# Optimization experiments

Hardware: AMD Instinct MI355X
Metric: run time of the kernel (lower is better)

## Reference

```python
import jax, jax.numpy as jnp
import numpy as np
import math

EPS = 1e-08
KERNEL = 3
PAD = KERNEL // 2


def setup_inputs() -> dict:
    key = jax.random.key(0)
    k1, k2, k3, k4 = jax.random.split(key, 4)
    B, C_in, C_out, H, W, S = 8, 512, 512, 64, 64, 512
    x = jax.random.normal(k1, (B, C_in, H, W), dtype=jnp.float32)
    style = jax.random.normal(k2, (B, S), dtype=jnp.float32)
    # modulation Linear: kaiming_normal fan_in linear => std = 1/sqrt(S); bias filled with 1
    w_mod = jax.random.normal(k3, (C_in, S), dtype=jnp.float32) / math.sqrt(S)
    b_mod = jnp.ones((C_in,), dtype=jnp.float32)
    # conv weight: randn / sqrt(in * k^2)
    weight = jax.random.normal(k4, (1, C_out, C_in, KERNEL, KERNEL), dtype=jnp.float32) / math.sqrt(C_in * KERNEL * KERNEL)
    return {"x": x, "style": style, "w_mod": w_mod, "b_mod": b_mod, "weight": weight}


def _modconv(x, style, w_mod, b_mod, weight):
    # style modulation: (B, S) @ (S, C_in) + bias -> (B, 1, C_in, 1, 1)
    s = style @ w_mod.T + b_mod
    w = weight * s[:, None, :, None, None]            # (B, C_out, C_in, k, k)
    # demodulate: rsqrt of sum of squares over (in, kh, kw)
    demod = jax.lax.rsqrt(jnp.sum(w * w, axis=(2, 3, 4)) + EPS)  # (B, C_out)
    w = w * demod[:, :, None, None, None]

    # groups=B conv == per-sample conv; vmap over batch
    def conv1(xb, wb):
        # xb: (C_in, H, W), wb: (C_out, C_in, k, k)
        return jax.lax.conv_general_dilated(
            xb[None], wb, window_strides=(1, 1),
            padding=[(PAD, PAD), (PAD, PAD)],
            dimension_numbers=("NCHW", "OIHW", "NCHW"))[0]

    return jax.vmap(conv1)(x, w)  # (B, C_out, H, W)


def reference(x, style, w_mod, b_mod, weight):
    return _modconv(x, style, w_mod, b_mod, weight)
```

## Files before the change

### kernel.cpp

```cpp
#include <hip/hip_runtime.h>
#include <hip/hip_bf16.h>

#define BATCH 8
#define CIN   512
#define COUT  512
#define HH    64
#define WW    64
#define SS    512
#define HP    66
#define WP    66
#define NPIX  (HH*WW)

typedef __bf16 bfrag  __attribute__((ext_vector_type(8)));
typedef float  f32x4  __attribute__((ext_vector_type(4)));
typedef unsigned short u16x8 __attribute__((ext_vector_type(8)));

__device__ __forceinline__ void async_copy16(const __hip_bfloat16* g, __hip_bfloat16* l) {
    __builtin_amdgcn_global_load_lds(
        (const __attribute__((address_space(1))) void*)g,
        (__attribute__((address_space(3))) void*)l,
        16, 0, 0);
}

__device__ __forceinline__ bool is_f32(const void* b_mod) {
    return ((const unsigned int*)b_mod)[0] == 0x3F800000u;
}

__global__ void k_prep(const void* __restrict__ style,
                       const void* __restrict__ w_mod,
                       const void* __restrict__ b_mod,
                       const void* __restrict__ weight,
                       float* __restrict__ s_out,
                       float* __restrict__ wsq,
                       __hip_bfloat16* __restrict__ Wt) {
    const bool f32 = is_f32(b_mod);
    if (blockIdx.x < 1024) {
        int tid = blockIdx.x * 256 + threadIdx.x;
        float sq = 0.f;
        if (f32) {
            const float* w = (const float*)weight + (size_t)tid * 9;
#pragma unroll
            for (int k = 0; k < 9; ++k) {
                float v = w[k];
                sq += v * v;
                Wt[k * (COUT * CIN) + tid] = __float2bfloat16(v);
            }
        } else {
            const __hip_bfloat16* w = (const __hip_bfloat16*)weight + (size_t)tid * 9;
#pragma unroll
            for (int k = 0; k < 9; ++k) {
                float v = __bfloat162float(w[k]);
                sq += v * v;
                Wt[k * (COUT * CIN) + tid] = w[k];
            }
        }
        wsq[tid] = sq;
    } else {
        int gw   = (blockIdx.x - 1024) * 4 + (threadIdx.x >> 6);
        int lane = threadIdx.x & 63;
        int b = gw >> 9, i = gw & 511;
        int base = lane * 8;
        float acc = 0.f;
        if (f32) {
            const float* st = (const float*)style + b * SS + base;
            const float* wm = (const float*)w_mod + i * SS + base;
#pragma unroll
            for (int j = 0; j < 8; ++j) acc += st[j] * wm[j];
        } else {
            const __hip_bfloat16* st = (const __hip_bfloat16*)style + b * SS + base;
            const __hip_bfloat16* wm = (const __hip_bfloat16*)w_mod + i * SS + base;
#pragma unroll
            for (int j = 0; j < 8; ++j)
                acc += __bfloat162float(st[j]) * __bfloat162float(wm[j]);
        }
#pragma unroll
        for (int off = 32; off; off >>= 1) acc += __shfl_down(acc, off);
        if (lane == 0) {
            float bias = f32 ? ((const float*)b_mod)[i]
                             : __bfloat162float(((const __hip_bfloat16*)b_mod)[i]);
            s_out[gw] = acc + bias;
        }
    }
}

__global__ void k_mid(const void* __restrict__ xv,
                      const float* __restrict__ s_buf,
                      const float* __restrict__ wsq,
                      const void* __restrict__ b_mod,
                      float* __restrict__ demod,
                      int b0, int nx, int do_demod,
                      __hip_bfloat16* __restrict__ xpad) {
    if ((int)blockIdx.x >= nx) {
        if (!do_demod) return;
        int gw   = ((int)blockIdx.x - nx) * 4 + (threadIdx.x >> 6);
        int lane = threadIdx.x & 63;
        int b = gw >> 9, o = gw & 511;
        int base = lane * 8;
        const float* sp = s_buf + b * CIN + base;
        const float* wp = wsq + o * CIN + base;
        float acc = 0.f;
#pragma unroll
        for (int j = 0; j < 8; ++j) {
            float sv = sp[j];
            acc += sv * sv * wp[j];
        }
#pragma unroll
        for (int off = 32; off; off >>= 1) acc += __shfl_down(acc, off);
        if (lane == 0) demod[gw] = rsqrtf(acc + 1e-8f);
        return;
    }
    const bool f32 = is_f32(b_mod);
    int ic = blockIdx.x & 15;
    int h  = (blockIdx.x >> 4) & 63;
    int bl = blockIdx.x >> 10;
    int b  = b0 + bl;
    int t  = threadIdx.x;
    int g  = t & 3;
    int w  = t >> 2;
    int ch0 = ic * 32 + g * 8;

    float sv[8];
#pragma unroll
    for (int j = 0; j < 8; ++j) sv[j] = s_buf[b * CIN + ch0 + j];

    u16x8 outv;
#pragma unroll
    for (int j = 0; j < 8; ++j) {
        size_t src = (size_t)(b * CIN + ch0 + j) * NPIX + h * WW + w;
        float xval = f32 ? ((const float*)xv)[src]
                         : __bfloat162float(((const __hip_bfloat16*)xv)[src]);
        __hip_bfloat16 bv = __float2bfloat16(xval * sv[j]);
        outv[j] = *(unsigned short*)&bv;
    }
    size_t rowb = (size_t)(bl * HP + h + 1) * WP;
    *(u16x8*)(xpad + (rowb + (w + 1)) * CIN + ch0) = outv;

    u16x8 z = {};
    if (w == 0)  *(u16x8*)(xpad + (rowb + 0)  * CIN + ch0) = z;
    if (w == 63) *(u16x8*)(xpad + (rowb + 65) * CIN + ch0) = z;
    if (h == 0) {
        size_t r0 = (size_t)(bl * HP + 0) * WP;
        *(u16x8*)(xpad + (r0 + (w + 1)) * CIN + ch0) = z;
        if (w == 0)  *(u16x8*)(xpad + (r0 + 0)  * CIN + ch0) = z;
        if (w == 63) *(u16x8*)(xpad + (r0 + 65) * CIN + ch0) = z;
    }
    if (h == 63) {
        size_t r65 = (size_t)(bl * HP + 65) * WP;
        *(u16x8*)(xpad + (r65 + (w + 1)) * CIN + ch0) = z;
        if (w == 0)  *(u16x8*)(xpad + (r65 + 0)  * CIN + ch0) = z;
        if (w == 63) *(u16x8*)(xpad + (r65 + 65) * CIN + ch0) = z;
    }
}

__global__ __launch_bounds__(512, 2)
void k_conv(const __hip_bfloat16* __restrict__ Wt,
            const __hip_bfloat16* __restrict__ xpad,
            const float* __restrict__ demod,
            const void* __restrict__ b_mod, int b0,
            void* __restrict__ outv) {
    __shared__ __hip_bfloat16 sA[2][3][256 * 32];
    __shared__ __hip_bfloat16 sB[2][384 * 32];

    const int tid  = threadIdx.x;
    const int wid  = tid >> 6;
    const int lane = tid & 63;

    const int id     = blockIdx.x;
    const int xcd    = id & 7;
    const int k      = id >> 3;
    const int o_tile = xcd >> 2;
    const int p_tile = (xcd & 3) * 4 + (k & 3);
    const int bl     = k >> 2;
    const int b      = b0 + bl;

    const int o_base = o_tile * 256;
    const int h0     = p_tile * 4;
    const int p_base = p_tile * 256;

    const int sw = ((lane & 3) ^ ((lane >> 3) & 3)) * 8;

    const int arow0 = wid * 32 + (lane >> 2);
    const int arow1 = arow0 + 16;
    const int aoff0 = wid * 1024 + lane * 8;
    const int aoff1 = aoff0 + 512;
    const int asrc0 = (o_base + arow0) * CIN + sw;
    const int asrc1 = (o_base + arow1) * CIN + sw;

    int bdst[3], bsrc[3];
#pragma unroll
    for (int jj = 0; jj < 3; ++jj) {
        int J   = wid * 3 + jj;
        int px  = J * 16 + (lane >> 2);
        int pm  = px < 263 ? px : 263;
        int r   = pm / 66;
        int c   = pm - r * 66;
        bdst[jj] = J * 512 + lane * 8;
        bsrc[jj] = ((bl * HP + h0 + r) * WP + c) * CIN + sw;
    }

    const int quad   = lane >> 4;
    const int l15    = lane & 15;
    const int wave_m = (wid >> 2) * 128;
    const int wave_n = (wid & 3) * 64;
    int afrag[8];
#pragma unroll
    for (int mt = 0; mt < 8; ++mt) {
        int row = wave_m + mt * 16 + l15;
        afrag[mt] = row * 32 + ((quad ^ ((l15 >> 1) & 3)) * 8);
    }
    int bfroff[4][3];
#pragma unroll
    for (int nt = 0; nt < 4; ++nt) {
        int n   = wave_n + nt * 16 + l15;
        int pr0 = (n >> 6) * 66 + (n & 63);
#pragma unroll
        for (int kw = 0; kw < 3; ++kw) {
            int pr = pr0 + kw;
            bfroff[nt][kw] = pr * 32 + ((quad ^ ((pr >> 1) & 3)) * 8);
        }
    }

    f32x4 acc[8][4];
#pragma unroll
    for (int mt = 0; mt < 8; ++mt)
#pragma unroll
        for (int nt = 0; nt < 4; ++nt)
            acc[mt][nt] = (f32x4)0.f;

    auto stageB = [&](int buf, int it) {
        const int kh = it >> 4;
        const int i0 = (it & 15) << 5;
        const __hip_bfloat16* xr = xpad + kh * (WP * CIN) + i0;
#pragma unroll
        for (int jj = 0; jj < 3; ++jj)
            async_copy16(xr + bsrc[jj], &sB[buf][bdst[jj]]);
    };
    auto stageA = [&](int buf, int it, int kw) {
        const int kh = it >> 4;
        const int i0 = (it & 15) << 5;
        const __hip_bfloat16* Ap = Wt + (kh * 3 + kw) * (COUT * CIN) + i0;
        async_copy16(Ap + asrc0, &sA[buf][kw][aoff0]);
        async_copy16(Ap + asrc1, &sA[buf][kw][aoff1]);
    };

    bfrag a[8], bb[4];
    auto ldfrags = [&](int buf, int kw) {
#pragma unroll
        for (int nt = 0; nt < 4; ++nt)
            bb[nt] = *(const bfrag*)(&sB[buf][bfroff[nt][kw]]);
#pragma unroll
        for (int mt = 0; mt < 8; ++mt)
            a[mt] = *(const bfrag*)(&sA[buf][kw][afrag[mt]]);
    };
    auto domfma = [&]() {
        __builtin_amdgcn_s_setprio(1);
#pragma unroll
        for (int mt = 0; mt < 8; ++mt)
#pragma unroll
            for (int nt = 0; nt < 4; ++nt)
                acc[mt][nt] = __builtin_amdgcn_mfma_f32_16x16x32_bf16(
                    a[mt], bb[nt], acc[mt][nt], 0, 0, 0);
        __builtin_amdgcn_s_setprio(0);
    };

#define PH(VMN, BUF, KW, STAGE_STMT)                                  \
    asm volatile("s_waitcnt vmcnt(" #VMN ")" ::: "memory");           \
    __builtin_amdgcn_s_barrier();                                     \
    asm volatile("" ::: "memory");                                    \
    ldfrags(BUF, KW);                                                 \
    STAGE_STMT;                                                       \
    __builtin_amdgcn_s_barrier();                                     \
    asm volatile("s_waitcnt lgkmcnt(0)" ::: "memory");                \
    __builtin_amdgcn_sched_barrier(0);                                \
    domfma();

    stageB(0, 0);
    stageA(0, 0, 0);
    stageA(0, 0, 1);
    stageA(0, 0, 2);

    for (int it = 0; it < 47; ++it) {
        const int buf = it & 1, nb = buf ^ 1, nit = it + 1;
        PH(4, buf, 0, stageB(nb, nit));
        PH(5, buf, 1, stageA(nb, nit, 0); stageA(nb, nit, 1));
        PH(7, buf, 2, stageA(nb, nit, 2));
    }
    PH(4, 1, 0, );
    PH(2, 1, 1, );
    PH(0, 1, 2, );
#undef PH

    const bool f32 = is_f32(b_mod);
#pragma unroll
    for (int mt = 0; mt < 8; ++mt) {
        const int o0r = o_base + wave_m + mt * 16 + quad * 4;
        float dm[4];
#pragma unroll
        for (int r = 0; r < 4; ++r) dm[r] = demod[b * COUT + o0r + r];
#pragma unroll
        for (int nt = 0; nt < 4; ++nt) {
            const int p = p_base + wave_n + nt * 16 + l15;
#pragma unroll
            for (int r = 0; r < 4; ++r) {
                float val = acc[mt][nt][r] * dm[r];
                size_t idx = (size_t)(b * COUT + o0r + r) * NPIX + p;
                if (f32) ((float*)outv)[idx] = val;
                else     ((__hip_bfloat16*)outv)[idx] = __float2bfloat16(val);
            }
        }
    }
}

extern "C" void kernel_launch(void* const* d_in, const int* in_sizes, int n_in,
                              void* d_out, int out_size, void* d_ws, size_t ws_size,
                              hipStream_t stream) {
    const void* x      = d_in[0];
    const void* style  = d_in[1];
    const void* w_mod  = d_in[2];
    const void* b_mod  = d_in[3];
    const void* weight = d_in[4];

    char* ws = (char*)d_ws;
    float*          s_buf = (float*)(ws + 4096);
    float*          demod = (float*)(ws + 20480);
    float*          wsq   = (float*)(ws + 36864);
    __hip_bfloat16* Wt    = (__hip_bfloat16*)(ws + 1085440);
    __hip_bfloat16* xpad  = (__hip_bfloat16*)(ws + 5804032);

    const size_t need_full = 5804032 + (size_t)BATCH * HP * WP * CIN * 2;
    const int group = (ws_size >= need_full) ? 8 : 4;

    k_prep<<<2048, 256, 0, stream>>>(style, w_mod, b_mod, weight, s_buf, wsq, Wt);

    for (int b0 = 0; b0 < BATCH; b0 += group) {
        const int nx = 1024 * group;
        const int do_demod = (b0 == 0) ? 1 : 0;
        const int nd = do_demod ? 1024 : 0;
        k_mid<<<nx + nd, 256, 0, stream>>>(x, s_buf, wsq, b_mod, demod,
                                           b0, nx, do_demod, xpad);
        k_conv<<<dim3(32 * group), 512, 0, stream>>>(Wt, xpad, demod, b_mod, b0, d_out);
    }
}
```

Before: 271.8 us.

## Split each kw phase into two half-M MFMA sub-phases with finer staging

Restructures the main loop so each kw phase is split into two halves of 4 M-tiles, loading A fragments per half and interleaving global-to-LDS async copies one at a time across six sub-phases instead of three. The aim is finer-grained overlap of LDS fragment loads and global prefetch with MFMA work, and smaller register live ranges for A fragments. In exchange it doubles the number of workgroup barriers per iteration, and the vmcnt wait counts had to be recomputed, which risks stalls or ordering mistakes.

```diff
diff --git a/kernel.cpp b/kernel.cpp
--- a/kernel.cpp
+++ b/kernel.cpp
@@ -202,12 +202,7 @@
     const int l15    = lane & 15;
     const int wave_m = (wid >> 2) * 128;
     const int wave_n = (wid & 3) * 64;
-    int afrag[8];
-#pragma unroll
-    for (int mt = 0; mt < 8; ++mt) {
-        int row = wave_m + mt * 16 + l15;
-        afrag[mt] = row * 32 + ((quad ^ ((l15 >> 1) & 3)) * 8);
-    }
+    const int afrag0 = (wave_m + l15) * 32 + ((quad ^ ((l15 >> 1) & 3)) * 8);
     int bfroff[4][3];
 #pragma unroll
     for (int nt = 0; nt < 4; ++nt) {
@@ -227,68 +222,85 @@
         for (int nt = 0; nt < 4; ++nt)
             acc[mt][nt] = (f32x4)0.f;
 
-    auto stageB = [&](int buf, int it) {
-        const int kh = it >> 4;
-        const int i0 = (it & 15) << 5;
-        const __hip_bfloat16* xr = xpad + kh * (WP * CIN) + i0;
-#pragma unroll
-        for (int jj = 0; jj < 3; ++jj)
-            async_copy16(xr + bsrc[jj], &sB[buf][bdst[jj]]);
-    };
-    auto stageA = [&](int buf, int it, int kw) {
-        const int kh = it >> 4;
-        const int i0 = (it & 15) << 5;
+    auto stageB1 = [&](int buf2, int it2, int jj) {
+        const int kh = it2 >> 4, i0 = (it2 & 15) << 5;
+        async_copy16(xpad + kh * (WP * CIN) + i0 + bsrc[jj], &sB[buf2][bdst[jj]]);
+    };
+    auto stageA2 = [&](int buf2, int it2, int kw) {
+        const int kh = it2 >> 4, i0 = (it2 & 15) << 5;
         const __hip_bfloat16* Ap = Wt + (kh * 3 + kw) * (COUT * CIN) + i0;
-        async_copy16(Ap + asrc0, &sA[buf][kw][aoff0]);
-        async_copy16(Ap + asrc1, &sA[buf][kw][aoff1]);
+        async_copy16(Ap + asrc0, &sA[buf2][kw][aoff0]);
+        async_copy16(Ap + asrc1, &sA[buf2][kw][aoff1]);
     };
 
     bfrag a[8], bb[4];
-    auto ldfrags = [&](int buf, int kw) {
+    auto ldB4 = [&](int buf2, int kw) {
 #pragma unroll
         for (int nt = 0; nt < 4; ++nt)
-            bb[nt] = *(const bfrag*)(&sB[buf][bfroff[nt][kw]]);
-#pragma unroll
-        for (int mt = 0; mt < 8; ++mt)
-            a[mt] = *(const bfrag*)(&sA[buf][kw][afrag[mt]]);
-    };
-    auto domfma = [&]() {
+            bb[nt] = *(const bfrag*)(&sB[buf2][bfroff[nt][kw]]);
+    };
+    auto ldA4 = [&](int buf2, int kw, int mh) {
+#pragma unroll
+        for (int m = 0; m < 4; ++m)
+            a[mh * 4 + m] = *(const bfrag*)(&sA[buf2][kw][afrag0 + (mh * 4 + m) * 512]);
+    };
+    auto mf16 = [&](int mh) {
         __builtin_amdgcn_s_setprio(1);
 #pragma unroll
-        for (int mt = 0; mt < 8; ++mt)
+        for (int m = 0; m < 4; ++m) {
+            const int mt = mh * 4 + m;
 #pragma unroll
             for (int nt = 0; nt < 4; ++nt)
                 acc[mt][nt] = __builtin_amdgcn_mfma_f32_16x16x32_bf16(
                     a[mt], bb[nt], acc[mt][nt], 0, 0, 0);
+        }
         __builtin_amdgcn_s_setprio(0);
     };
 
-#define PH(VMN, BUF, KW, STAGE_STMT)                                  \
-    asm volatile("s_waitcnt vmcnt(" #VMN ")" ::: "memory");           \
-    __builtin_amdgcn_s_barrier();                                     \
-    asm volatile("" ::: "memory");                                    \
-    ldfrags(BUF, KW);                                                 \
-    STAGE_STMT;                                                       \
+#define PRE                                                           \
     __builtin_amdgcn_s_barrier();                                     \
     asm volatile("s_waitcnt lgkmcnt(0)" ::: "memory");                \
-    __builtin_amdgcn_sched_barrier(0);                                \
-    domfma();
-
-    stageB(0, 0);
-    stageA(0, 0, 0);
-    stageA(0, 0, 1);
-    stageA(0, 0, 2);
+    __builtin_amdgcn_sched_barrier(0)
+#define WAITV(N) asm volatile("s_waitcnt vmcnt(" #N ")" ::: "memory")
+#define POST                                                          \
+    __builtin_amdgcn_s_barrier();                                     \
+    asm volatile("" ::: "memory")
+
+    stageB1(0, 0, 0); stageB1(0, 0, 1); stageB1(0, 0, 2);
+    stageA2(0, 0, 0); stageA2(0, 0, 1); stageA2(0, 0, 2);
+    WAITV(4);
+    POST;
 
     for (int it = 0; it < 47; ++it) {
         const int buf = it & 1, nb = buf ^ 1, nit = it + 1;
-        PH(4, buf, 0, stageB(nb, nit));
-        PH(5, buf, 1, stageA(nb, nit, 0); stageA(nb, nit, 1));
-        PH(7, buf, 2, stageA(nb, nit, 2));
-    }
-    PH(4, 1, 0, );
-    PH(2, 1, 1, );
-    PH(0, 1, 2, );
-#undef PH
+        ldB4(buf, 0); ldA4(buf, 0, 0); stageB1(nb, nit, 0);
+        PRE; mf16(0); POST;
+        ldA4(buf, 0, 1); stageB1(nb, nit, 1);
+        PRE; mf16(1); WAITV(4); POST;
+        ldB4(buf, 1); ldA4(buf, 1, 0); stageB1(nb, nit, 2);
+        PRE; mf16(0); POST;
+        ldA4(buf, 1, 1); stageA2(nb, nit, 0);
+        PRE; mf16(1); WAITV(5); POST;
+        ldB4(buf, 2); ldA4(buf, 2, 0); stageA2(nb, nit, 1);
+        PRE; mf16(0); POST;
+        ldA4(buf, 2, 1); stageA2(nb, nit, 2);
+        PRE; mf16(1); WAITV(4); POST;
+    }
+    ldB4(1, 0); ldA4(1, 0, 0);
+    PRE; mf16(0); POST;
+    ldA4(1, 0, 1);
+    PRE; mf16(1); WAITV(2); POST;
+    ldB4(1, 1); ldA4(1, 1, 0);
+    PRE; mf16(0); POST;
+    ldA4(1, 1, 1);
+    PRE; mf16(1); WAITV(0); POST;
+    ldB4(1, 2); ldA4(1, 2, 0);
+    PRE; mf16(0); POST;
+    ldA4(1, 2, 1);
+    PRE; mf16(1); POST;
+#undef PRE
+#undef WAITV
+#undef POST
 
     const bool f32 = is_f32(b_mod);
 #pragma unroll
```

After: 262.1 us. 1.04x faster.
